# Kernel tuning notes

Measured on AMD Instinct MI355X. Metric: run time of the kernel, lower is better.

The kernel has to match this reference:

```python
import jax, jax.numpy as jnp
import numpy as np

NUM_POS = 4
N = 8192
C = 4096  # number of identity classes == logit dim


def setup_inputs() -> dict:
    key = jax.random.key(0)
    k1, k2 = jax.random.split(key)
    feat = jax.random.normal(k1, (N, C), dtype=jnp.float32)
    label = jax.random.randint(k2, (N,), 0, C, dtype=jnp.int64)
    return {"feat": feat, "label": label}


def reference(feat, label):
    # feat: [n, C] logits, label: [n] int class ids.
    n, c = feat.shape
    # Segment-mean replaces the O(n^2) masked-mean loop:
    # center[i] = mean of feat over all j with label[j] == label[i]
    sums = jax.ops.segment_sum(feat, label, num_segments=c)              # [C, C]
    counts = jax.ops.segment_sum(jnp.ones((n,), feat.dtype), label,
                                 num_segments=c)                          # [C]
    center = sums[label] / counts[label][:, None]                         # [n, C]
    # CrossEntropyLoss (mean reduction) on centers as logits
    logp = jax.nn.log_softmax(center, axis=-1)
    ce = -jnp.take_along_axis(logp, label[:, None], axis=1)[:, 0].mean()
    m = n / NUM_POS
    return ce / m
```

## Files before the change

### kernel.cpp

```cpp
#include <hip/hip_runtime.h>
#include <math.h>

#define NN 8192
#define CC 4096
#define SLOTS 64
#define BLK 256
#define NSPLIT 16

#define SCALE (4.0f / (8192.0f * 8192.0f))

__global__ void init_kernel(int* __restrict__ counts, float* __restrict__ out) {
    int i = blockIdx.x * blockDim.x + threadIdx.x;
    if (i < CC) counts[i] = 0;
    if (i == 0) out[0] = 0.0f;
}

__global__ void build_index(const int* __restrict__ label,
                            int* __restrict__ counts,
                            int* __restrict__ lists) {
    int i = blockIdx.x * blockDim.x + threadIdx.x;
    if (i < NN) {
        int lab = label[i];
        int pos = atomicAdd(&counts[lab], 1);
        if (pos < SLOTS) lists[lab * SLOTS + pos] = i;
    }
}

template <int T>
__device__ inline float4 gather_sum(const float4* __restrict__ feat4,
                                    const int* __restrict__ rl, int m, int slot) {
    int r0 = rl[0];
    float4 v[T];
    #pragma unroll
    for (int k = 0; k < T; ++k) {
        int r = (k < m) ? rl[k] : r0;
        v[k] = feat4[(size_t)r * (CC / 4) + slot];
    }
    float4 a = make_float4(0.f, 0.f, 0.f, 0.f);
    #pragma unroll
    for (int k = 0; k < T; ++k) {
        float w = (k < m) ? 1.f : 0.f;
        a.x += w * v[k].x; a.y += w * v[k].y; a.z += w * v[k].z; a.w += w * v[k].w;
    }
    return a;
}

__global__ __launch_bounds__(BLK) void part_kernel(const float4* __restrict__ feat4,
                                                   const int* __restrict__ counts,
                                                   const int* __restrict__ lists,
                                                   float4* __restrict__ part) {
    int lane = threadIdx.x & 63;
    int wv = __builtin_amdgcn_readfirstlane(threadIdx.x >> 6);
    int task = blockIdx.x * 4 + wv;
    int c = task >> 4;
    int s = task & 15;

    int cnt = counts[c];
    if (cnt == 0) return;
    int m = cnt < SLOTS ? cnt : SLOTS;

    const int* rl = lists + c * SLOTS;
    int slot = s * 64 + lane;

    float4 acc;
    if (m <= 2)      acc = gather_sum<2>(feat4, rl, m, slot);
    else if (m <= 4) acc = gather_sum<4>(feat4, rl, m, slot);
    else if (m <= 8) acc = gather_sum<8>(feat4, rl, m, slot);
    else {
        acc = gather_sum<16>(feat4, rl, m, slot);
        for (int k = 16; k < m; ++k) {
            float4 v = feat4[(size_t)rl[k] * (CC / 4) + slot];
            acc.x += v.x; acc.y += v.y; acc.z += v.z; acc.w += v.w;
        }
    }

    float inv = 1.0f / (float)cnt;
    float mean[4] = {acc.x * inv, acc.y * inv, acc.z * inv, acc.w * inv};

    float M = fmaxf(fmaxf(mean[0], mean[1]), fmaxf(mean[2], mean[3]));
    #pragma unroll
    for (int off = 1; off < 64; off <<= 1) M = fmaxf(M, __shfl_xor(M, off, 64));

    float S = __expf(mean[0] - M) + __expf(mean[1] - M) +
              __expf(mean[2] - M) + __expf(mean[3] - M);
    #pragma unroll
    for (int off = 1; off < 64; off <<= 1) S += __shfl_xor(S, off, 64);

    float cand = mean[c & 3];
    float vcown = __shfl(cand, (c >> 2) & 63, 64);
    float vc = (s == (c >> 8)) ? vcown : 0.f;

    if (lane == 0) part[s * CC + c] = make_float4(M, S, vc, 0.f);
}

__global__ __launch_bounds__(BLK) void finalize(const float4* __restrict__ part,
                                                const int* __restrict__ counts,
                                                float* __restrict__ out) {
    int c = blockIdx.x * BLK + threadIdx.x;
    int cnt = counts[c];
    float contrib = 0.f;
    if (cnt > 0) {
        float4 p[NSPLIT];
        #pragma unroll
        for (int s = 0; s < NSPLIT; ++s) p[s] = part[s * CC + c];
        float M = p[0].x;
        #pragma unroll
        for (int s = 1; s < NSPLIT; ++s) M = fmaxf(M, p[s].x);
        float S = 0.f, vc = 0.f;
        #pragma unroll
        for (int s = 0; s < NSPLIT; ++s) {
            S += p[s].y * __expf(p[s].x - M);
            vc += p[s].z;
        }
        contrib = (float)cnt * (M + __logf(S) - vc);
    }

    #pragma unroll
    for (int off = 1; off < 64; off <<= 1) contrib += __shfl_xor(contrib, off, 64);
    __shared__ float s_red[4];
    int lane = threadIdx.x & 63, w = threadIdx.x >> 6;
    if (lane == 0) s_red[w] = contrib;
    __syncthreads();
    if (threadIdx.x == 0)
        atomicAdd(out, (s_red[0] + s_red[1] + s_red[2] + s_red[3]) * SCALE);
}

extern "C" void kernel_launch(void* const* d_in, const int* in_sizes, int n_in,
                              void* d_out, int out_size, void* d_ws, size_t ws_size,
                              hipStream_t stream) {
    const float* feat = (const float*)d_in[0];
    const int* label = (const int*)d_in[1];
    float* out = (float*)d_out;

    int* counts = (int*)d_ws;
    int* lists = counts + CC;
    float4* part = (float4*)(lists + CC * SLOTS);

    init_kernel<<<(CC + BLK - 1) / BLK, BLK, 0, stream>>>(counts, out);
    build_index<<<(NN + BLK - 1) / BLK, BLK, 0, stream>>>(label, counts, lists);
    part_kernel<<<CC * NSPLIT / 4, BLK, 0, stream>>>((const float4*)feat, counts, lists, part);
    finalize<<<CC / BLK, BLK, 0, stream>>>(part, counts, out);
}
```

Baseline: 198.9 us.

## Process one class per 512-thread block and drop split partials

Replaces the 16-way split per class (one wave per slice, partials written to global) with one 512-thread block per class. Each thread gathers two float4 columns, and the softmax max, sum and target logit are reduced through shared memory. This removes the partial buffer and the merge in finalize. Finalize becomes a single block that sums per-class contributions and stores the result directly instead of using atomics. The aim is less global traffic and fewer waves, at the cost of block-level syncs and less parallelism per class.

Result: slower. 207.3 us (+4.2%).

```diff
diff --git a/kernel.cpp b/kernel.cpp
--- a/kernel.cpp
+++ b/kernel.cpp
@@ -4,15 +4,14 @@
 #define NN 8192
 #define CC 4096
 #define SLOTS 64
-#define BLK 256
-#define NSPLIT 16
+#define CB 512
+#define NF4 (CC / 4)
 
 #define SCALE (4.0f / (8192.0f * 8192.0f))
 
-__global__ void init_kernel(int* __restrict__ counts, float* __restrict__ out) {
+__global__ void init_kernel(int* __restrict__ counts) {
     int i = blockIdx.x * blockDim.x + threadIdx.x;
     if (i < CC) counts[i] = 0;
-    if (i == 0) out[0] = 0.0f;
 }
 
 __global__ void build_index(const int* __restrict__ label,
@@ -27,102 +26,102 @@
 }
 
 template <int T>
-__device__ inline float4 gather_sum(const float4* __restrict__ feat4,
-                                    const int* __restrict__ rl, int m, int slot) {
+__device__ inline void gather2(const float4* __restrict__ feat4,
+                               const int* __restrict__ rl, int m,
+                               int s0, int s1, float4& a0, float4& a1) {
     int r0 = rl[0];
-    float4 v[T];
+    float4 v0[T], v1[T];
     #pragma unroll
     for (int k = 0; k < T; ++k) {
         int r = (k < m) ? rl[k] : r0;
-        v[k] = feat4[(size_t)r * (CC / 4) + slot];
+        size_t rb = (size_t)r * NF4;
+        v0[k] = feat4[rb + s0];
+        v1[k] = feat4[rb + s1];
     }
-    float4 a = make_float4(0.f, 0.f, 0.f, 0.f);
     #pragma unroll
     for (int k = 0; k < T; ++k) {
         float w = (k < m) ? 1.f : 0.f;
-        a.x += w * v[k].x; a.y += w * v[k].y; a.z += w * v[k].z; a.w += w * v[k].w;
+        a0.x += w * v0[k].x; a0.y += w * v0[k].y; a0.z += w * v0[k].z; a0.w += w * v0[k].w;
+        a1.x += w * v1[k].x; a1.y += w * v1[k].y; a1.z += w * v1[k].z; a1.w += w * v1[k].w;
     }
-    return a;
 }
 
-__global__ __launch_bounds__(BLK) void part_kernel(const float4* __restrict__ feat4,
-                                                   const int* __restrict__ counts,
-                                                   const int* __restrict__ lists,
-                                                   float4* __restrict__ part) {
-    int lane = threadIdx.x & 63;
-    int wv = __builtin_amdgcn_readfirstlane(threadIdx.x >> 6);
-    int task = blockIdx.x * 4 + wv;
-    int c = task >> 4;
-    int s = task & 15;
+__global__ __launch_bounds__(CB) void center_kernel(const float4* __restrict__ feat4,
+                                                    const int* __restrict__ counts,
+                                                    const int* __restrict__ lists,
+                                                    float* __restrict__ contrib) {
+    int c = blockIdx.x;
+    int t = threadIdx.x;
+    int cnt = counts[c];
+    if (cnt == 0) {
+        if (t == 0) contrib[c] = 0.f;
+        return;
+    }
+    int m = cnt < SLOTS ? cnt : SLOTS;
+    const int* rl = lists + c * SLOTS;
 
-    int cnt = counts[c];
-    if (cnt == 0) return;
-    int m = cnt < SLOTS ? cnt : SLOTS;
-
-    const int* rl = lists + c * SLOTS;
-    int slot = s * 64 + lane;
-
-    float4 acc;
-    if (m <= 2)      acc = gather_sum<2>(feat4, rl, m, slot);
-    else if (m <= 4) acc = gather_sum<4>(feat4, rl, m, slot);
-    else if (m <= 8) acc = gather_sum<8>(feat4, rl, m, slot);
+    float4 a0 = make_float4(0.f, 0.f, 0.f, 0.f);
+    float4 a1 = make_float4(0.f, 0.f, 0.f, 0.f);
+    if (m == 1)      gather2<1>(feat4, rl, m, t, t + CB, a0, a1);
+    else if (m == 2) gather2<2>(feat4, rl, m, t, t + CB, a0, a1);
+    else if (m <= 4) gather2<4>(feat4, rl, m, t, t + CB, a0, a1);
     else {
-        acc = gather_sum<16>(feat4, rl, m, slot);
-        for (int k = 16; k < m; ++k) {
-            float4 v = feat4[(size_t)rl[k] * (CC / 4) + slot];
-            acc.x += v.x; acc.y += v.y; acc.z += v.z; acc.w += v.w;
+        gather2<8>(feat4, rl, m < 8 ? m : 8, t, t + CB, a0, a1);
+        for (int k = 8; k < m; ++k) {
+            size_t rb = (size_t)rl[k] * NF4;
+            float4 v0 = feat4[rb + t], v1 = feat4[rb + t + CB];
+            a0.x += v0.x; a0.y += v0.y; a0.z += v0.z; a0.w += v0.w;
+            a1.x += v1.x; a1.y += v1.y; a1.z += v1.z; a1.w += v1.w;
         }
     }
 
     float inv = 1.0f / (float)cnt;
-    float mean[4] = {acc.x * inv, acc.y * inv, acc.z * inv, acc.w * inv};
+    float e0[4] = {a0.x * inv, a0.y * inv, a0.z * inv, a0.w * inv};
+    float e1[4] = {a1.x * inv, a1.y * inv, a1.z * inv, a1.w * inv};
 
-    float M = fmaxf(fmaxf(mean[0], mean[1]), fmaxf(mean[2], mean[3]));
+    __shared__ float s_m[CB / 64], s_s[CB / 64], s_v;
+    int lane = t & 63, w = t >> 6;
+
+    float M = fmaxf(fmaxf(fmaxf(e0[0], e0[1]), fmaxf(e0[2], e0[3])),
+                    fmaxf(fmaxf(e1[0], e1[1]), fmaxf(e1[2], e1[3])));
     #pragma unroll
     for (int off = 1; off < 64; off <<= 1) M = fmaxf(M, __shfl_xor(M, off, 64));
+    if (lane == 0) s_m[w] = M;
 
-    float S = __expf(mean[0] - M) + __expf(mean[1] - M) +
-              __expf(mean[2] - M) + __expf(mean[3] - M);
+    int sIdx = c >> 2;
+    if (t == (sIdx & (CB - 1))) s_v = (sIdx < CB) ? e0[c & 3] : e1[c & 3];
+    __syncthreads();
+
+    M = s_m[0];
+    #pragma unroll
+    for (int j = 1; j < CB / 64; ++j) M = fmaxf(M, s_m[j]);
+
+    float S = __expf(e0[0] - M) + __expf(e0[1] - M) + __expf(e0[2] - M) + __expf(e0[3] - M)
+            + __expf(e1[0] - M) + __expf(e1[1] - M) + __expf(e1[2] - M) + __expf(e1[3] - M);
     #pragma unroll
     for (int off = 1; off < 64; off <<= 1) S += __shfl_xor(S, off, 64);
+    if (lane == 0) s_s[w] = S;
+    __syncthreads();
 
-    float cand = mean[c & 3];
-    float vcown = __shfl(cand, (c >> 2) & 63, 64);
-    float vc = (s == (c >> 8)) ? vcown : 0.f;
-
-    if (lane == 0) part[s * CC + c] = make_float4(M, S, vc, 0.f);
+    if (t == 0) {
+        float Stot = 0.f;
+        #pragma unroll
+        for (int j = 0; j < CB / 64; ++j) Stot += s_s[j];
+        contrib[c] = (float)cnt * (M + __logf(Stot) - s_v);
+    }
 }
 
-__global__ __launch_bounds__(BLK) void finalize(const float4* __restrict__ part,
-                                                const int* __restrict__ counts,
+__global__ __launch_bounds__(256) void finalize(const float* __restrict__ contrib,
                                                 float* __restrict__ out) {
-    int c = blockIdx.x * BLK + threadIdx.x;
-    int cnt = counts[c];
-    float contrib = 0.f;
-    if (cnt > 0) {
-        float4 p[NSPLIT];
-        #pragma unroll
-        for (int s = 0; s < NSPLIT; ++s) p[s] = part[s * CC + c];
-        float M = p[0].x;
-        #pragma unroll
-        for (int s = 1; s < NSPLIT; ++s) M = fmaxf(M, p[s].x);
-        float S = 0.f, vc = 0.f;
-        #pragma unroll
-        for (int s = 0; s < NSPLIT; ++s) {
-            S += p[s].y * __expf(p[s].x - M);
-            vc += p[s].z;
-        }
-        contrib = (float)cnt * (M + __logf(S) - vc);
-    }
-
+    float s = 0.f;
+    for (int i = threadIdx.x; i < CC; i += 256) s += contrib[i];
     #pragma unroll
-    for (int off = 1; off < 64; off <<= 1) contrib += __shfl_xor(contrib, off, 64);
-    __shared__ float s_red[4];
+    for (int off = 1; off < 64; off <<= 1) s += __shfl_xor(s, off, 64);
+    __shared__ float sr[4];
     int lane = threadIdx.x & 63, w = threadIdx.x >> 6;
-    if (lane == 0) s_red[w] = contrib;
+    if (lane == 0) sr[w] = s;
     __syncthreads();
-    if (threadIdx.x == 0)
-        atomicAdd(out, (s_red[0] + s_red[1] + s_red[2] + s_red[3]) * SCALE);
+    if (threadIdx.x == 0) out[0] = (sr[0] + sr[1] + sr[2] + sr[3]) * SCALE;
 }
 
 extern "C" void kernel_launch(void* const* d_in, const int* in_sizes, int n_in,
@@ -134,10 +133,10 @@
 
     int* counts = (int*)d_ws;
     int* lists = counts + CC;
-    float4* part = (float4*)(lists + CC * SLOTS);
+    float* contrib = (float*)(lists + CC * SLOTS);
 
-    init_kernel<<<(CC + BLK - 1) / BLK, BLK, 0, stream>>>(counts, out);
-    build_index<<<(NN + BLK - 1) / BLK, BLK, 0, stream>>>(label, counts, lists);
-    part_kernel<<<CC * NSPLIT / 4, BLK, 0, stream>>>((const float4*)feat, counts, lists, part);
-    finalize<<<CC / BLK, BLK, 0, stream>>>(part, counts, out);
+    init_kernel<<<(CC + 255) / 256, 256, 0, stream>>>(counts);
+    build_index<<<(NN + 255) / 256, 256, 0, stream>>>(label, counts, lists);
+    center_kernel<<<CC, CB, 0, stream>>>((const float4*)feat, counts, lists, contrib);
+    finalize<<<1, 256, 0, stream>>>(contrib, out);
 }
```
